# Kernel optimization log

Measured on AMD Instinct MI355X. Metric: run time of the kernel, lower is better.

The kernel has to match this reference:

```python
import jax, jax.numpy as jnp
import numpy as np

ITERATIONS = 3

def setup_inputs() -> dict:
    key = jax.random.key(0)
    k1, k2 = jax.random.split(key)
    C, S, H = 64, 128, 2048
    x = jax.random.normal(k1, (C, S, H), dtype=jnp.float32)
    W = jax.random.normal(k2, (H, H), dtype=jnp.float32)
    return {"x": x, "W": W}

def reference(x, W):
    # x: [C, S, H], W: [H, H]
    C, S, H = x.shape
    # e_ij is loop-invariant in the original; hoist it (same math, computed once)
    e_ij = jnp.einsum('csh,hk->csk', x, W)  # [C, S, H]
    b_ij = jnp.zeros((C, S), dtype=x.dtype)
    c_i = jnp.zeros((C, H), dtype=x.dtype)
    for _ in range(ITERATIONS):
        d_i = jax.nn.softmax(b_ij, axis=1)[:, :, None]          # [C, S, 1], softmax over S
        c_i = jnp.sum(d_i * e_ij, axis=1)                        # [C, H]
        squared = jnp.sum(c_i ** 2, axis=1, keepdims=True)       # [C, 1]
        coeff = squared / (1.0 + squared) / jnp.sqrt(squared + 1e-9)
        c_i = coeff * c_i                                        # squash
        b_ij = b_ij + jnp.einsum('csh,ch->cs', e_ij, c_i)        # logit update
    return c_i
```

## Files before the change

### kernel.cpp

```cpp
#include <hip/hip_runtime.h>

using bf16x8 = __attribute__((ext_vector_type(8))) __bf16;
using f32x4  = __attribute__((ext_vector_type(4))) float;

#define C_ 64
#define S_ 128
#define H_ 2048
#define M_ 8192

__device__ __forceinline__ unsigned short f2bf(float f) {
  unsigned u = __float_as_uint(f);
  u = u + 0x7fffu + ((u >> 16) & 1u);
  return (unsigned short)(u >> 16);
}
__device__ __forceinline__ float bf2f(unsigned short h) {
  return __uint_as_float(((unsigned)h) << 16);
}

__device__ __forceinline__ void glds16(const unsigned short* g, unsigned short* l) {
  __builtin_amdgcn_global_load_lds(
      (const __attribute__((address_space(1))) void*)g,
      (__attribute__((address_space(3))) void*)l, 16, 0, 0);
}

__global__ void k_split_all(const float* __restrict__ x,
                            unsigned short* __restrict__ xh,
                            unsigned short* __restrict__ xl,
                            const float* __restrict__ W,
                            unsigned short* __restrict__ Wth,
                            unsigned short* __restrict__ Wtl,
                            float* __restrict__ G) {
  __shared__ float Ts[64][68];
  const int b = blockIdx.x;
  const int t = threadIdx.x;
  if (b < 16384) {
    int idx = b * 256 + t;
    float4 v = ((const float4*)x)[idx];
    float a[4] = {v.x, v.y, v.z, v.w};
    unsigned short h[4], l[4];
#pragma unroll
    for (int q = 0; q < 4; ++q) {
      h[q] = f2bf(a[q]);
      l[q] = f2bf(a[q] - bf2f(h[q]));
    }
    ((ushort4*)xh)[idx] = make_ushort4(h[0], h[1], h[2], h[3]);
    ((ushort4*)xl)[idx] = make_ushort4(l[0], l[1], l[2], l[3]);
  } else if (b < 17408) {
    const int bb = b - 16384;
    const int k0 = (bb & 31) * 64, n0 = (bb >> 5) * 64;
#pragma unroll
    for (int p = 0; p < 4; ++p) {
      int idx = t + p * 256;
      int r = idx >> 4, c4 = (idx & 15) * 4;
      *(float4*)&Ts[r][c4] = *(const float4*)(W + (size_t)(k0 + r) * H_ + n0 + c4);
    }
    __syncthreads();
#pragma unroll
    for (int p = 0; p < 4; ++p) {
      int idx = t + p * 256;
      int rr = idx >> 4, cc = (idx & 15) * 4;
      unsigned short h[4], l[4];
#pragma unroll
      for (int q = 0; q < 4; ++q) {
        float f = Ts[cc + q][rr];
        h[q] = f2bf(f);
        l[q] = f2bf(f - bf2f(h[q]));
      }
      size_t o = (size_t)(n0 + rr) * H_ + k0 + cc;
      *(ushort4*)(Wth + o) = make_ushort4(h[0], h[1], h[2], h[3]);
      *(ushort4*)(Wtl + o) = make_ushort4(l[0], l[1], l[2], l[3]);
    }
  } else {
    const int bb = b - 17408;
    ((float4*)G)[bb * 256 + t] = (float4){0.f, 0.f, 0.f, 0.f};
  }
}

#define TILE_USH 24576
#define OFF_AH 0
#define OFF_AL 8192
#define OFF_BH 16384
#define OFF_BL 20480

__global__ __launch_bounds__(512, 2) void k_gemm3(
    const unsigned short* __restrict__ Ah, const unsigned short* __restrict__ Al,
    const unsigned short* __restrict__ Bh, const unsigned short* __restrict__ Bl,
    unsigned short* __restrict__ Eh, unsigned short* __restrict__ El) {
  __shared__ unsigned short lds[3 * TILE_USH];
  const int t = threadIdx.x;
  const int lane = t & 63, wid = t >> 6;
  const int wm = wid >> 1, wn = wid & 1;
  const int l16 = lane & 15, quad = lane >> 4;

  const int lin = blockIdx.x + (blockIdx.y << 5);
  const int xcd = lin & 7, slot = lin >> 3;
  const int bm = ((xcd >> 1) << 3) + (slot >> 3);
  const int bn = ((xcd & 1) << 3) + (slot & 7);

  const int rl = lane >> 2;
  const int gg8 = (((lane & 3) ^ ((rl >> 1) & 3)) << 3);
  const unsigned short* gAh0 = Ah + (size_t)(bm * 256 + wid * 16 + rl) * H_ + gg8;
  const unsigned short* gAl0 = Al + (size_t)(bm * 256 + wid * 16 + rl) * H_ + gg8;
  const unsigned short* gAh1 = gAh0 + (size_t)128 * H_;
  const unsigned short* gAl1 = gAl0 + (size_t)128 * H_;
  const unsigned short* gBh  = Bh + (size_t)(bn * 128 + wid * 16 + rl) * H_ + gg8;
  const unsigned short* gBl  = Bl + (size_t)(bn * 128 + wid * 16 + rl) * H_ + gg8;
  const int dA0 = wid * 512;
  const int dA1 = dA0 + 4096;
  const int dB  = wid * 512;

  const int colq = ((quad ^ ((l16 >> 1) & 3)) << 3);
  const int rA = (wm * 64 + l16) * 32 + colq;
  const int rB = (wn * 64 + l16) * 32 + colq;

  f32x4 acc[4][4];
#pragma unroll
  for (int i = 0; i < 4; ++i)
#pragma unroll
    for (int j = 0; j < 4; ++j) acc[i][j] = (f32x4)0.f;

  auto stage6 = [&](int bo, int k) {
    glds16(gAh0 + k, &lds[bo + OFF_AH + dA0]);
    glds16(gAh1 + k, &lds[bo + OFF_AH + dA1]);
    glds16(gAl0 + k, &lds[bo + OFF_AL + dA0]);
    glds16(gAl1 + k, &lds[bo + OFF_AL + dA1]);
    glds16(gBh + k,  &lds[bo + OFF_BH + dB]);
    glds16(gBl + k,  &lds[bo + OFF_BL + dB]);
  };

  stage6(0, 0);
  stage6(TILE_USH, 32);
  asm volatile("s_waitcnt vmcnt(6)" ::: "memory");
  __builtin_amdgcn_s_barrier();

  int cur = 0;
#pragma unroll 1
  for (int tt = 0; tt < 64; ++tt) {
    const int co = cur * TILE_USH;
    bf16x8 ah[4], al[4], bh[4], bl[4];
#pragma unroll
    for (int i = 0; i < 4; ++i) {
      ah[i] = *(const bf16x8*)&lds[co + OFF_AH + rA + i * 512];
      al[i] = *(const bf16x8*)&lds[co + OFF_AL + rA + i * 512];
      bh[i] = *(const bf16x8*)&lds[co + OFF_BH + rB + i * 512];
      bl[i] = *(const bf16x8*)&lds[co + OFF_BL + rB + i * 512];
    }
    if (tt < 62) {
      int n2 = cur + 2; if (n2 >= 3) n2 -= 3;
      stage6(n2 * TILE_USH, (tt + 2) * 32);
    }
    __builtin_amdgcn_s_setprio(1);
#pragma unroll
    for (int i = 0; i < 4; ++i)
#pragma unroll
      for (int j = 0; j < 4; ++j) {
        acc[i][j] = __builtin_amdgcn_mfma_f32_16x16x32_bf16(ah[i], bh[j], acc[i][j], 0, 0, 0);
        acc[i][j] = __builtin_amdgcn_mfma_f32_16x16x32_bf16(ah[i], bl[j], acc[i][j], 0, 0, 0);
        acc[i][j] = __builtin_amdgcn_mfma_f32_16x16x32_bf16(al[i], bh[j], acc[i][j], 0, 0, 0);
      }
    __builtin_amdgcn_s_setprio(0);
    if (tt < 62)       asm volatile("s_waitcnt vmcnt(6)" ::: "memory");
    else if (tt == 62) asm volatile("s_waitcnt vmcnt(0)" ::: "memory");
    if (tt < 63) __builtin_amdgcn_s_barrier();
    cur = cur + 1; if (cur == 3) cur = 0;
  }

#pragma unroll
  for (int i = 0; i < 4; ++i) {
    const int row0 = bm * 256 + wm * 64 + i * 16 + quad * 4;
#pragma unroll
    for (int j = 0; j < 4; ++j) {
      const int col = bn * 128 + wn * 64 + j * 16 + l16;
#pragma unroll
      for (int r = 0; r < 4; ++r) {
        float v = acc[i][j][r];
        unsigned short hh = f2bf(v);
        unsigned short ll = f2bf(v - bf2f(hh));
        Eh[(size_t)(row0 + r) * H_ + col] = hh;
        El[(size_t)(row0 + r) * H_ + col] = ll;
      }
    }
  }
}

__global__ __launch_bounds__(256, 4) void k_gram_mfma(
    const unsigned short* __restrict__ Eh, const unsigned short* __restrict__ El,
    float* __restrict__ G) {
  __shared__ unsigned short sH[128 * 32], sL[128 * 32];
  const int t = threadIdx.x;
  const int kc = blockIdx.x;
  const int cc = blockIdx.y;
  const int lane = t & 63, wid = t >> 6;
  const int wm = wid >> 1, wn = wid & 1;
  const int l16 = lane & 15, quad = lane >> 4;

  const int rl = lane >> 2;
  const int gg = (lane & 3) ^ ((rl >> 1) & 3);
  const int c0 = wid * 2, c1 = c0 + 1;
  const unsigned short* gH0 = Eh + (size_t)(cc * 128 + c0 * 16 + rl) * H_ + gg * 8;
  const unsigned short* gH1 = Eh + (size_t)(cc * 128 + c1 * 16 + rl) * H_ + gg * 8;
  const unsigned short* gL0 = El + (size_t)(cc * 128 + c0 * 16 + rl) * H_ + gg * 8;
  const unsigned short* gL1 = El + (size_t)(cc * 128 + c1 * 16 + rl) * H_ + gg * 8;
  unsigned short* lH0 = sH + c0 * 512;
  unsigned short* lH1 = sH + c1 * 512;
  unsigned short* lL0 = sL + c0 * 512;
  unsigned short* lL1 = sL + c1 * 512;

  const int swz = ((l16 >> 1) & 3);
  const int colq = ((quad ^ swz) * 8);

  f32x4 acc[4][4];
#pragma unroll
  for (int i = 0; i < 4; ++i)
#pragma unroll
    for (int j = 0; j < 4; ++j) acc[i][j] = (f32x4)0.f;

  const int kbeg = kc * 512;
  for (int k0 = kbeg; k0 < kbeg + 512; k0 += 32) {
    __syncthreads();
    glds16(gH0 + k0, lH0);
    glds16(gH1 + k0, lH1);
    glds16(gL0 + k0, lL0);
    glds16(gL1 + k0, lL1);
    __syncthreads();

    bf16x8 ah[4], al[4], bh[4], bl[4];
#pragma unroll
    for (int i = 0; i < 4; ++i) {
      const int ra = (wm * 64 + i * 16 + l16) * 32;
      const int rb = (wn * 64 + i * 16 + l16) * 32;
      ah[i] = *(const bf16x8*)&sH[ra + colq];
      al[i] = *(const bf16x8*)&sL[ra + colq];
      bh[i] = *(const bf16x8*)&sH[rb + colq];
      bl[i] = *(const bf16x8*)&sL[rb + colq];
    }
#pragma unroll
    for (int i = 0; i < 4; ++i)
#pragma unroll
      for (int j = 0; j < 4; ++j) {
        acc[i][j] = __builtin_amdgcn_mfma_f32_16x16x32_bf16(ah[i], bh[j], acc[i][j], 0, 0, 0);
        acc[i][j] = __builtin_amdgcn_mfma_f32_16x16x32_bf16(ah[i], bl[j], acc[i][j], 0, 0, 0);
        acc[i][j] = __builtin_amdgcn_mfma_f32_16x16x32_bf16(al[i], bh[j], acc[i][j], 0, 0, 0);
      }
  }

  float* Gc = G + (size_t)cc * S_ * S_;
#pragma unroll
  for (int i = 0; i < 4; ++i) {
    const int row0 = wm * 64 + i * 16 + quad * 4;
#pragma unroll
    for (int j = 0; j < 4; ++j) {
      const int col = wn * 64 + j * 16 + l16;
#pragma unroll
      for (int r = 0; r < 4; ++r)
        atomicAdd(&Gc[(row0 + r) * S_ + col], acc[i][j][r]);
    }
  }
}

__global__ void k_out2(const unsigned short* __restrict__ Eh,
                       const unsigned short* __restrict__ El,
                       const float* __restrict__ G, float* __restrict__ out) {
  const int c = blockIdx.y;
  const int s = threadIdx.x & 127;
  __shared__ float dsh[128];
  __shared__ float red[128];
  __shared__ float wsh[128];
  const float* Gc = G + (size_t)c * S_ * S_;
  float b = 0.f;
  for (int it = 0; it < 3; ++it) {
    red[s] = b; __syncthreads();
    for (int off = 64; off > 0; off >>= 1) {
      if (s < off) red[s] = fmaxf(red[s], red[s + off]);
      __syncthreads();
    }
    float mx = red[0]; __syncthreads();
    float ev = expf(b - mx);
    red[s] = ev; __syncthreads();
    for (int off = 64; off > 0; off >>= 1) {
      if (s < off) red[s] = red[s] + red[s + off];
      __syncthreads();
    }
    float Z = red[0]; __syncthreads();
    float d = ev / Z;
    dsh[s] = d; __syncthreads();
    float y = 0.f;
#pragma unroll 8
    for (int j = 0; j < S_; ++j) y = fmaf(Gc[j * S_ + s], dsh[j], y);
    red[s] = d * y; __syncthreads();
    for (int off = 64; off > 0; off >>= 1) {
      if (s < off) red[s] = red[s] + red[s + off];
      __syncthreads();
    }
    float sq = red[0]; __syncthreads();
    float coeff = sq / (1.f + sq) / sqrtf(sq + 1e-9f);
    if (it == 2) wsh[s] = coeff * d;
    else b += coeff * y;
  }
  __syncthreads();

  const int h2 = blockIdx.x * 256 + threadIdx.x;
  const unsigned* Ph = (const unsigned*)(Eh + (size_t)c * S_ * H_) + h2;
  const unsigned* Pl = (const unsigned*)(El + (size_t)c * S_ * H_) + h2;
  float a0 = 0.f, a1 = 0.f;
#pragma unroll 8
  for (int ss = 0; ss < S_; ++ss) {
    unsigned uh = Ph[(size_t)ss * (H_ / 2)];
    unsigned ul = Pl[(size_t)ss * (H_ / 2)];
    a0 = fmaf(wsh[ss], bf2f((unsigned short)uh) + bf2f((unsigned short)ul), a0);
    a1 = fmaf(wsh[ss], bf2f((unsigned short)(uh >> 16)) + bf2f((unsigned short)(ul >> 16)), a1);
  }
  ((float2*)(out + (size_t)c * H_))[h2] = make_float2(a0, a1);
}

extern "C" void kernel_launch(void* const* d_in, const int* in_sizes, int n_in,
                              void* d_out, int out_size, void* d_ws, size_t ws_size,
                              hipStream_t stream) {
  (void)in_sizes; (void)n_in; (void)out_size; (void)ws_size;
  const float* x = (const float*)d_in[0];
  const float* W = (const float*)d_in[1];
  float* out = (float*)d_out;
  char* ws = (char*)d_ws;

  unsigned short* xh  = (unsigned short*)(ws);
  unsigned short* xl  = (unsigned short*)(ws + 33554432);
  unsigned short* Wth = (unsigned short*)(ws + 67108864);
  unsigned short* Wtl = (unsigned short*)(ws + 75497472);
  unsigned short* Eh  = (unsigned short*)(ws + 83886080);
  unsigned short* El  = (unsigned short*)(ws + 117440512);
  float*          G   = (float*)(ws + 150994944);

  k_split_all<<<dim3(18432), 256, 0, stream>>>(x, xh, xl, W, Wth, Wtl, G);
  k_gemm3<<<dim3(32, 16), 512, 0, stream>>>(xh, xl, Wth, Wtl, Eh, El);
  k_gram_mfma<<<dim3(4, 64), 256, 0, stream>>>(Eh, El, G);
  k_out2<<<dim3(4, 64), 256, 0, stream>>>(Eh, El, G, out);
}
```

Measured before the change: 342.9 us.

## Double-buffer LDS fragment registers to overlap LDS reads with MFMA in GEMM

Restructures the k_gemm3 main loop into a 2x-unrolled ping-pong, where LDS fragments for the next K-step load into a second register set while MFMAs run on the current set. Global-to-LDS staging is reordered so each stage is issued before the barrier, and sched_barriers pin the instruction order. The aim is to hide LDS read latency behind matrix math. It doubles fragment register use, which may pressure VGPRs at 2 waves per SIMD, and the ring-buffer bookkeeping is delicate.

```diff
diff --git a/kernel.cpp b/kernel.cpp
--- a/kernel.cpp
+++ b/kernel.cpp
@@ -82,6 +82,29 @@
 #define OFF_BH 16384
 #define OFF_BL 20480
 
+#define LOADSET(AH, AL, BH, BL, off)                                  \
+  do {                                                                \
+    const int _o = (off);                                             \
+    _Pragma("unroll") for (int i = 0; i < 4; ++i) {                   \
+      AH[i] = *(const bf16x8*)&lds[_o + OFF_AH + rA + i * 512];       \
+      AL[i] = *(const bf16x8*)&lds[_o + OFF_AL + rA + i * 512];       \
+      BH[i] = *(const bf16x8*)&lds[_o + OFF_BH + rB + i * 512];       \
+      BL[i] = *(const bf16x8*)&lds[_o + OFF_BL + rB + i * 512];       \
+    }                                                                 \
+  } while (0)
+
+#define MFMASET(AH, AL, BH, BL)                                                                  \
+  do {                                                                                           \
+    __builtin_amdgcn_s_setprio(1);                                                               \
+    _Pragma("unroll") for (int i = 0; i < 4; ++i)                                                \
+        _Pragma("unroll") for (int j = 0; j < 4; ++j) {                                          \
+      acc[i][j] = __builtin_amdgcn_mfma_f32_16x16x32_bf16(AH[i], BH[j], acc[i][j], 0, 0, 0);     \
+      acc[i][j] = __builtin_amdgcn_mfma_f32_16x16x32_bf16(AH[i], BL[j], acc[i][j], 0, 0, 0);     \
+      acc[i][j] = __builtin_amdgcn_mfma_f32_16x16x32_bf16(AL[i], BH[j], acc[i][j], 0, 0, 0);     \
+    }                                                                                            \
+    __builtin_amdgcn_s_setprio(0);                                                               \
+  } while (0)
+
 __global__ __launch_bounds__(512, 2) void k_gemm3(
     const unsigned short* __restrict__ Ah, const unsigned short* __restrict__ Al,
     const unsigned short* __restrict__ Bh, const unsigned short* __restrict__ Bl,
@@ -132,38 +155,41 @@
   stage6(TILE_USH, 32);
   asm volatile("s_waitcnt vmcnt(6)" ::: "memory");
   __builtin_amdgcn_s_barrier();
-
-  int cur = 0;
+  __builtin_amdgcn_sched_barrier(0);
+
+  bf16x8 ahA[4], alA[4], bhA[4], blA[4];
+  bf16x8 ahB[4], alB[4], bhB[4], blB[4];
+  LOADSET(ahA, alA, bhA, blA, 0);
+
+  int stage_off = 2 * TILE_USH;
+  int read_off  = TILE_USH;
+
 #pragma unroll 1
-  for (int tt = 0; tt < 64; ++tt) {
-    const int co = cur * TILE_USH;
-    bf16x8 ah[4], al[4], bh[4], bl[4];
-#pragma unroll
-    for (int i = 0; i < 4; ++i) {
-      ah[i] = *(const bf16x8*)&lds[co + OFF_AH + rA + i * 512];
-      al[i] = *(const bf16x8*)&lds[co + OFF_AL + rA + i * 512];
-      bh[i] = *(const bf16x8*)&lds[co + OFF_BH + rB + i * 512];
-      bl[i] = *(const bf16x8*)&lds[co + OFF_BL + rB + i * 512];
-    }
-    if (tt < 62) {
-      int n2 = cur + 2; if (n2 >= 3) n2 -= 3;
-      stage6(n2 * TILE_USH, (tt + 2) * 32);
-    }
-    __builtin_amdgcn_s_setprio(1);
-#pragma unroll
-    for (int i = 0; i < 4; ++i)
-#pragma unroll
-      for (int j = 0; j < 4; ++j) {
-        acc[i][j] = __builtin_amdgcn_mfma_f32_16x16x32_bf16(ah[i], bh[j], acc[i][j], 0, 0, 0);
-        acc[i][j] = __builtin_amdgcn_mfma_f32_16x16x32_bf16(ah[i], bl[j], acc[i][j], 0, 0, 0);
-        acc[i][j] = __builtin_amdgcn_mfma_f32_16x16x32_bf16(al[i], bh[j], acc[i][j], 0, 0, 0);
-      }
-    __builtin_amdgcn_s_setprio(0);
-    if (tt < 62)       asm volatile("s_waitcnt vmcnt(6)" ::: "memory");
-    else if (tt == 62) asm volatile("s_waitcnt vmcnt(0)" ::: "memory");
-    if (tt < 63) __builtin_amdgcn_s_barrier();
-    cur = cur + 1; if (cur == 3) cur = 0;
-  }
+  for (int tt = 0; tt < 62; tt += 2) {
+    stage6(stage_off, (tt + 2) * 32);
+    stage_off += TILE_USH; if (stage_off == 3 * TILE_USH) stage_off = 0;
+    asm volatile("s_waitcnt vmcnt(6) lgkmcnt(0)" ::: "memory");
+    __builtin_amdgcn_s_barrier();
+    __builtin_amdgcn_sched_barrier(0);
+    LOADSET(ahB, alB, bhB, blB, read_off);
+    read_off += TILE_USH; if (read_off == 3 * TILE_USH) read_off = 0;
+    MFMASET(ahA, alA, bhA, blA);
+    stage6(stage_off, (tt + 3) * 32);
+    stage_off += TILE_USH; if (stage_off == 3 * TILE_USH) stage_off = 0;
+    asm volatile("s_waitcnt vmcnt(6) lgkmcnt(0)" ::: "memory");
+    __builtin_amdgcn_s_barrier();
+    __builtin_amdgcn_sched_barrier(0);
+    LOADSET(ahA, alA, bhA, blA, read_off);
+    read_off += TILE_USH; if (read_off == 3 * TILE_USH) read_off = 0;
+    MFMASET(ahB, alB, bhB, blB);
+  }
+
+  asm volatile("s_waitcnt vmcnt(0) lgkmcnt(0)" ::: "memory");
+  __builtin_amdgcn_s_barrier();
+  __builtin_amdgcn_sched_barrier(0);
+  LOADSET(ahB, alB, bhB, blB, read_off);
+  MFMASET(ahA, alA, bhA, blA);
+  MFMASET(ahB, alB, bhB, blB);
 
 #pragma unroll
   for (int i = 0; i < 4; ++i) {
```

Result: no change. 339.9 us (-0.9%).

## Enlarge GEMM tile to 256x256 with double buffering; double-buffer gram kernel loads

Applied to the files above, without the earlier changes.

The main split-bf16 GEMM moves from 256x128 tiles with a 3-stage LDS pipeline to 256x256 tiles with 2-stage buffering. Each wave now computes 128x64 outputs and A fragments are loaded per row block, which raises operand reuse and halves the grid to 256 blocks. The gram kernel switches from two syncs per K step to a double-buffered prefetch with raised priority around the MFMAs. In exchange, the GEMM has more accumulator registers per thread, a shallower prefetch, and fewer blocks than there are CUs, which risks lower occupancy and idle units.

```diff
diff --git a/kernel.cpp b/kernel.cpp
--- a/kernel.cpp
+++ b/kernel.cpp
@@ -76,26 +76,26 @@
   }
 }
 
-#define TILE_USH 24576
+#define TILE_USH 32768
 #define OFF_AH 0
 #define OFF_AL 8192
 #define OFF_BH 16384
-#define OFF_BL 20480
+#define OFF_BL 24576
 
 __global__ __launch_bounds__(512, 2) void k_gemm3(
     const unsigned short* __restrict__ Ah, const unsigned short* __restrict__ Al,
     const unsigned short* __restrict__ Bh, const unsigned short* __restrict__ Bl,
     unsigned short* __restrict__ Eh, unsigned short* __restrict__ El) {
-  __shared__ unsigned short lds[3 * TILE_USH];
+  __shared__ unsigned short lds[2 * TILE_USH];
   const int t = threadIdx.x;
   const int lane = t & 63, wid = t >> 6;
-  const int wm = wid >> 1, wn = wid & 1;
+  const int wm = wid >> 2, wn = wid & 3;
   const int l16 = lane & 15, quad = lane >> 4;
 
   const int lin = blockIdx.x + (blockIdx.y << 5);
   const int xcd = lin & 7, slot = lin >> 3;
-  const int bm = ((xcd >> 1) << 3) + (slot >> 3);
-  const int bn = ((xcd & 1) << 3) + (slot & 7);
+  const int bm = xcd * 4 + (slot >> 3);
+  const int bn = slot & 7;
 
   const int rl = lane >> 2;
   const int gg8 = (((lane & 3) ^ ((rl >> 1) & 3)) << 3);
@@ -103,74 +103,77 @@
   const unsigned short* gAl0 = Al + (size_t)(bm * 256 + wid * 16 + rl) * H_ + gg8;
   const unsigned short* gAh1 = gAh0 + (size_t)128 * H_;
   const unsigned short* gAl1 = gAl0 + (size_t)128 * H_;
-  const unsigned short* gBh  = Bh + (size_t)(bn * 128 + wid * 16 + rl) * H_ + gg8;
-  const unsigned short* gBl  = Bl + (size_t)(bn * 128 + wid * 16 + rl) * H_ + gg8;
+  const unsigned short* gBh0 = Bh + (size_t)(bn * 256 + wid * 16 + rl) * H_ + gg8;
+  const unsigned short* gBl0 = Bl + (size_t)(bn * 256 + wid * 16 + rl) * H_ + gg8;
+  const unsigned short* gBh1 = gBh0 + (size_t)128 * H_;
+  const unsigned short* gBl1 = gBl0 + (size_t)128 * H_;
   const int dA0 = wid * 512;
   const int dA1 = dA0 + 4096;
-  const int dB  = wid * 512;
+  const int dB0 = wid * 512;
+  const int dB1 = dB0 + 4096;
 
   const int colq = ((quad ^ ((l16 >> 1) & 3)) << 3);
-  const int rA = (wm * 64 + l16) * 32 + colq;
+  const int rA = (wm * 128 + l16) * 32 + colq;
   const int rB = (wn * 64 + l16) * 32 + colq;
 
-  f32x4 acc[4][4];
-#pragma unroll
-  for (int i = 0; i < 4; ++i)
+  f32x4 acc[8][4];
+#pragma unroll
+  for (int i = 0; i < 8; ++i)
 #pragma unroll
     for (int j = 0; j < 4; ++j) acc[i][j] = (f32x4)0.f;
 
-  auto stage6 = [&](int bo, int k) {
+  auto stage8 = [&](int bo, int k) {
     glds16(gAh0 + k, &lds[bo + OFF_AH + dA0]);
     glds16(gAh1 + k, &lds[bo + OFF_AH + dA1]);
     glds16(gAl0 + k, &lds[bo + OFF_AL + dA0]);
     glds16(gAl1 + k, &lds[bo + OFF_AL + dA1]);
-    glds16(gBh + k,  &lds[bo + OFF_BH + dB]);
-    glds16(gBl + k,  &lds[bo + OFF_BL + dB]);
+    glds16(gBh0 + k, &lds[bo + OFF_BH + dB0]);
+    glds16(gBh1 + k, &lds[bo + OFF_BH + dB1]);
+    glds16(gBl0 + k, &lds[bo + OFF_BL + dB0]);
+    glds16(gBl1 + k, &lds[bo + OFF_BL + dB1]);
   };
 
-  stage6(0, 0);
-  stage6(TILE_USH, 32);
-  asm volatile("s_waitcnt vmcnt(6)" ::: "memory");
+  stage8(0, 0);
+  asm volatile("s_waitcnt vmcnt(0)" ::: "memory");
   __builtin_amdgcn_s_barrier();
 
   int cur = 0;
 #pragma unroll 1
   for (int tt = 0; tt < 64; ++tt) {
     const int co = cur * TILE_USH;
-    bf16x8 ah[4], al[4], bh[4], bl[4];
-#pragma unroll
-    for (int i = 0; i < 4; ++i) {
-      ah[i] = *(const bf16x8*)&lds[co + OFF_AH + rA + i * 512];
-      al[i] = *(const bf16x8*)&lds[co + OFF_AL + rA + i * 512];
-      bh[i] = *(const bf16x8*)&lds[co + OFF_BH + rB + i * 512];
-      bl[i] = *(const bf16x8*)&lds[co + OFF_BL + rB + i * 512];
-    }
-    if (tt < 62) {
-      int n2 = cur + 2; if (n2 >= 3) n2 -= 3;
-      stage6(n2 * TILE_USH, (tt + 2) * 32);
+    if (tt < 63) stage8((cur ^ 1) * TILE_USH, (tt + 1) * 32);
+    bf16x8 bh[4], bl[4];
+#pragma unroll
+    for (int j = 0; j < 4; ++j) {
+      bh[j] = *(const bf16x8*)&lds[co + OFF_BH + rB + j * 512];
+      bl[j] = *(const bf16x8*)&lds[co + OFF_BL + rB + j * 512];
     }
     __builtin_amdgcn_s_setprio(1);
 #pragma unroll
-    for (int i = 0; i < 4; ++i)
+    for (int i = 0; i < 8; ++i) {
+      bf16x8 ah = *(const bf16x8*)&lds[co + OFF_AH + rA + i * 512];
+      bf16x8 al = *(const bf16x8*)&lds[co + OFF_AL + rA + i * 512];
 #pragma unroll
       for (int j = 0; j < 4; ++j) {
-        acc[i][j] = __builtin_amdgcn_mfma_f32_16x16x32_bf16(ah[i], bh[j], acc[i][j], 0, 0, 0);
-        acc[i][j] = __builtin_amdgcn_mfma_f32_16x16x32_bf16(ah[i], bl[j], acc[i][j], 0, 0, 0);
-        acc[i][j] = __builtin_amdgcn_mfma_f32_16x16x32_bf16(al[i], bh[j], acc[i][j], 0, 0, 0);
+        acc[i][j] = __builtin_amdgcn_mfma_f32_16x16x32_bf16(ah, bh[j], acc[i][j], 0, 0, 0);
+        acc[i][j] = __builtin_amdgcn_mfma_f32_16x16x32_bf16(ah, bl[j], acc[i][j], 0, 0, 0);
+        acc[i][j] = __builtin_amdgcn_mfma_f32_16x16x32_bf16(al, bh[j], acc[i][j], 0, 0, 0);
       }
+    }
     __builtin_amdgcn_s_setprio(0);
-    if (tt < 62)       asm volatile("s_waitcnt vmcnt(6)" ::: "memory");
-    else if (tt == 62) asm volatile("s_waitcnt vmcnt(0)" ::: "memory");
-    if (tt < 63) __builtin_amdgcn_s_barrier();
-    cur = cur + 1; if (cur == 3) cur = 0;
-  }
-
-#pragma unroll
-  for (int i = 0; i < 4; ++i) {
-    const int row0 = bm * 256 + wm * 64 + i * 16 + quad * 4;
+    if (tt < 63) {
+      asm volatile("s_waitcnt vmcnt(0) lgkmcnt(0)" ::: "memory");
+      __builtin_amdgcn_s_barrier();
+    }
+    cur ^= 1;
+  }
+
+#pragma unroll
+  for (int i = 0; i < 8; ++i) {
+    const int row0 = bm * 256 + wm * 128 + i * 16 + quad * 4;
 #pragma unroll
     for (int j = 0; j < 4; ++j) {
-      const int col = bn * 128 + wn * 64 + j * 16 + l16;
+      const int col = bn * 256 + wn * 64 + j * 16 + l16;
 #pragma unroll
       for (int r = 0; r < 4; ++r) {
         float v = acc[i][j][r];
@@ -186,7 +189,7 @@
 __global__ __launch_bounds__(256, 4) void k_gram_mfma(
     const unsigned short* __restrict__ Eh, const unsigned short* __restrict__ El,
     float* __restrict__ G) {
-  __shared__ unsigned short sH[128 * 32], sL[128 * 32];
+  __shared__ unsigned short sb[2][16384];
   const int t = threadIdx.x;
   const int kc = blockIdx.x;
   const int cc = blockIdx.y;
@@ -201,10 +204,7 @@
   const unsigned short* gH1 = Eh + (size_t)(cc * 128 + c1 * 16 + rl) * H_ + gg * 8;
   const unsigned short* gL0 = El + (size_t)(cc * 128 + c0 * 16 + rl) * H_ + gg * 8;
   const unsigned short* gL1 = El + (size_t)(cc * 128 + c1 * 16 + rl) * H_ + gg * 8;
-  unsigned short* lH0 = sH + c0 * 512;
-  unsigned short* lH1 = sH + c1 * 512;
-  unsigned short* lL0 = sL + c0 * 512;
-  unsigned short* lL1 = sL + c1 * 512;
+  const int dH0 = c0 * 512, dH1 = c1 * 512;
 
   const int swz = ((l16 >> 1) & 3);
   const int colq = ((quad ^ swz) * 8);
@@ -215,15 +215,24 @@
 #pragma unroll
     for (int j = 0; j < 4; ++j) acc[i][j] = (f32x4)0.f;
 
+  auto stage4 = [&](int buf, int k) {
+    glds16(gH0 + k, &sb[buf][dH0]);
+    glds16(gH1 + k, &sb[buf][dH1]);
+    glds16(gL0 + k, &sb[buf][8192 + dH0]);
+    glds16(gL1 + k, &sb[buf][8192 + dH1]);
+  };
+
   const int kbeg = kc * 512;
-  for (int k0 = kbeg; k0 < kbeg + 512; k0 += 32) {
-    __syncthreads();
-    glds16(gH0 + k0, lH0);
-    glds16(gH1 + k0, lH1);
-    glds16(gL0 + k0, lL0);
-    glds16(gL1 + k0, lL1);
-    __syncthreads();
-
+  stage4(0, kbeg);
+  asm volatile("s_waitcnt vmcnt(0)" ::: "memory");
+  __builtin_amdgcn_s_barrier();
+
+  int cur = 0;
+#pragma unroll 1
+  for (int s = 0; s < 16; ++s) {
+    if (s < 15) stage4(cur ^ 1, kbeg + (s + 1) * 32);
+    const unsigned short* sH = &sb[cur][0];
+    const unsigned short* sL = &sb[cur][8192];
     bf16x8 ah[4], al[4], bh[4], bl[4];
 #pragma unroll
     for (int i = 0; i < 4; ++i) {
@@ -234,6 +243,7 @@
       bh[i] = *(const bf16x8*)&sH[rb + colq];
       bl[i] = *(const bf16x8*)&sL[rb + colq];
     }
+    __builtin_amdgcn_s_setprio(1);
 #pragma unroll
     for (int i = 0; i < 4; ++i)
 #pragma unroll
@@ -242,6 +252,12 @@
         acc[i][j] = __builtin_amdgcn_mfma_f32_16x16x32_bf16(ah[i], bl[j], acc[i][j], 0, 0, 0);
         acc[i][j] = __builtin_amdgcn_mfma_f32_16x16x32_bf16(al[i], bh[j], acc[i][j], 0, 0, 0);
       }
+    __builtin_amdgcn_s_setprio(0);
+    if (s < 15) {
+      asm volatile("s_waitcnt vmcnt(0) lgkmcnt(0)" ::: "memory");
+      __builtin_amdgcn_s_barrier();
+    }
+    cur ^= 1;
   }
 
   float* Gc = G + (size_t)cc * S_ * S_;
@@ -331,7 +347,7 @@
   float*          G   = (float*)(ws + 150994944);
 
   k_split_all<<<dim3(18432), 256, 0, stream>>>(x, xh, xl, W, Wth, Wtl, G);
-  k_gemm3<<<dim3(32, 16), 512, 0, stream>>>(xh, xl, Wth, Wtl, Eh, El);
+  k_gemm3<<<dim3(32, 8), 512, 0, stream>>>(xh, xl, Wth, Wtl, Eh, El);
   k_gram_mfma<<<dim3(4, 64), 256, 0, stream>>>(Eh, El, G);
   k_out2<<<dim3(4, 64), 256, 0, stream>>>(Eh, El, G, out);
 }
```

Result: faster. 323.0 us (-5.8%).
